# Optimization experiments

Measured on AMD Instinct MI355X. Metric: run time of the kernel, lower is better.

Reference implementation:

```python
import jax, jax.numpy as jnp
import numpy as np

B, N, E = 256, 10000, 160000
H1, H2 = 1024, 128


def setup_inputs() -> dict:
    key = jax.random.key(0)
    ks = jax.random.split(key, 8)
    data = jax.random.normal(ks[0], (B, N), dtype=jnp.float32)
    edge_index = jax.random.randint(ks[1], (2, E), 0, N, dtype=jnp.int64)
    # GCNConv(1, 1): scalar weight + scalar bias (Glorot-ish init)
    gcn_w = jax.random.normal(ks[2], (1,), dtype=jnp.float32)
    gcn_b = jnp.zeros((1,), dtype=jnp.float32)
    # encoder: Linear(N, 1024) -> ReLU -> Linear(1024, 128) -> ReLU
    W1 = jax.random.normal(ks[3], (N, H1), dtype=jnp.float32) * (1.0 / np.sqrt(N))
    b1 = jnp.zeros((H1,), dtype=jnp.float32)
    W2 = jax.random.normal(ks[4], (H1, H2), dtype=jnp.float32) * (1.0 / np.sqrt(H1))
    b2 = jnp.zeros((H2,), dtype=jnp.float32)
    return {"data": data, "gcn_w": gcn_w, "gcn_b": gcn_b,
            "W1": W1, "b1": b1, "W2": W2, "b2": b2,
            "edge_index": edge_index}


def reference(data, gcn_w, gcn_b, W1, b1, W2, b2, edge_index):
    n = data.shape[1]
    # PyG GCNConv defaults: add self-loops, symmetric normalization.
    loop = jnp.arange(n, dtype=edge_index.dtype)
    src = jnp.concatenate([edge_index[0], loop])  # [E+N]
    dst = jnp.concatenate([edge_index[1], loop])
    deg = jax.ops.segment_sum(jnp.ones_like(dst, dtype=data.dtype), dst,
                              num_segments=n)  # >= 1 thanks to self-loops
    dinv = jax.lax.rsqrt(deg)
    norm = dinv[src] * dinv[dst]  # [E+N]
    # linear on 1-dim node features == scalar multiply, batched over B samples
    xw = data * gcn_w[0]                      # [B, N]
    msgs = xw[:, src] * norm                  # [B, E+N]
    agg = jax.ops.segment_sum(msgs.T, dst, num_segments=n).T  # [B, N]
    g = jax.nn.relu(agg + gcn_b[0])           # relu'd GCN output, one row per sample
    # dense MLP encoder (p_drop = 0 so dropout is identity)
    h = jax.nn.relu(g @ W1 + b1)              # [B, 1024]
    return jax.nn.relu(h @ W2 + b2)           # [B, 128]
```

## Files before the change

kernel.cpp:

```cpp
#include <hip/hip_runtime.h>
#include <hip/hip_bf16.h>


#define KPAD 10240
#define NSTEPS 20
#define ZSPLIT 16
#define ELLW 64

typedef __attribute__((ext_vector_type(8))) short short8v;
typedef __attribute__((ext_vector_type(4))) float f32x4;

__device__ inline short f2bf(float f) {
    union { float f; unsigned u; } v; v.f = f;
    unsigned r = v.u + 0x7fffu + ((v.u >> 16) & 1u);
    return (short)(r >> 16);
}

__device__ inline float bf2f(short s) {
    union { unsigned u; float f; } v;
    v.u = ((unsigned)(unsigned short)s) << 16;
    return v.f;
}

__device__ inline void gll16(const short* g, short* l) {
    __builtin_amdgcn_global_load_lds(
        (const __attribute__((address_space(1))) void*)g,
        (__attribute__((address_space(3))) void*)l, 16, 0, 0);
}

__global__ void pack_kernel(const float* __restrict__ data, const float* __restrict__ gw,
                            short* __restrict__ xwT, const float* __restrict__ W1,
                            short* __restrict__ W1T, float4* __restrict__ cntz,
                            int N, int B, int H1, int tTiles, int cTiles) {
    __shared__ short tile[32][66];
    int id = blockIdx.x, t = threadIdx.x;
    if (id < tTiles) {
        int nt = (N + 31) >> 5;
        int xb = id % nt, yb = id / nt;
        int n0 = xb * 32, b0 = yb * 32;
        float w = gw[0];
        int tx = t & 31, ty = t >> 5;
#pragma unroll
        for (int i = 0; i < 4; ++i) {
            int b = b0 + ty + i * 8;
            int n = n0 + tx;
            float v = (n < N) ? data[(size_t)b * N + n] : 0.f;
            tile[ty + i * 8][tx] = f2bf(v * w);
        }
        __syncthreads();
#pragma unroll
        for (int i = 0; i < 4; ++i) {
            int n = n0 + ty + i * 8;
            if (n < N) xwT[(size_t)n * B + b0 + tx] = tile[tx][ty + i * 8];
        }
    } else if (id < tTiles + cTiles) {
        int c = id - tTiles;
        int nk = KPAD >> 6;
        int kx = c % nk, hy = c / nk;
        int k0 = kx * 64, h0 = hy * 32;
        int hl = t & 31, kr = t >> 5;
#pragma unroll
        for (int i = 0; i < 8; ++i) {
            int k = k0 + kr + i * 8;
            float v = (k < N) ? W1[(size_t)k * H1 + h0 + hl] : 0.f;
            tile[hl][kr + i * 8] = f2bf(v);
        }
        __syncthreads();
        int kl = t & 63, hr = t >> 6;
#pragma unroll
        for (int i = 0; i < 8; ++i) {
            int h = h0 + hr + i * 4;
            W1T[(size_t)h * KPAD + k0 + kl] = tile[hr + i * 4][kl];
        }
    } else {
        int i = (id - tTiles - cTiles) * 256 + t;
        cntz[i] = make_float4(0.f, 0.f, 0.f, 0.f);
    }
}

__global__ void ell_fill(const int* __restrict__ ei, int* __restrict__ cnt,
                         int* __restrict__ ell, int E) {
    int e = blockIdx.x * blockDim.x + threadIdx.x;
    if (e >= E) return;
    int s = ei[e], d = ei[E + e];
    int c = atomicAdd(&cnt[d], 1);
    if (c < ELLW) ell[(d << 6) + c] = s;
}

__global__ void gather_kernel(const int* __restrict__ cnt, const int* __restrict__ ell,
                              const float* __restrict__ gcn_b, const short* __restrict__ xwT,
                              short* __restrict__ A0, int N, int B) {
    int row = blockIdx.x * 4 + (threadIdx.x >> 6);
    if (row >= N) return;
    int lane = threadIdx.x & 63;
    const short4* x4 = (const short4*)xwT;
    const int B4 = B >> 2;
    float gb = gcn_b[0];
    int dcnt = cnt[row];
    float di = rsqrtf((float)dcnt + 1.0f);
    float w = di * di;
    short4 v = x4[(size_t)row * B4 + lane];
    float ax = bf2f(v.x) * w, ay = bf2f(v.y) * w, az = bf2f(v.z) * w, aw = bf2f(v.w) * w;
    const int* er = ell + ((size_t)row << 6);
    int m = dcnt < ELLW ? dcnt : ELLW;
    int i = 0;
    for (; i + 1 < m; i += 2) {
        int s0 = er[i], s1 = er[i + 1];
        float n0 = rsqrtf((float)cnt[s0] + 1.0f) * di;
        float n1 = rsqrtf((float)cnt[s1] + 1.0f) * di;
        short4 u0 = x4[(size_t)s0 * B4 + lane];
        short4 u1 = x4[(size_t)s1 * B4 + lane];
        ax = fmaf(bf2f(u0.x), n0, ax); ay = fmaf(bf2f(u0.y), n0, ay);
        az = fmaf(bf2f(u0.z), n0, az); aw = fmaf(bf2f(u0.w), n0, aw);
        ax = fmaf(bf2f(u1.x), n1, ax); ay = fmaf(bf2f(u1.y), n1, ay);
        az = fmaf(bf2f(u1.z), n1, az); aw = fmaf(bf2f(u1.w), n1, aw);
    }
    if (i < m) {
        int s0 = er[i];
        float n0 = rsqrtf((float)cnt[s0] + 1.0f) * di;
        short4 u0 = x4[(size_t)s0 * B4 + lane];
        ax = fmaf(bf2f(u0.x), n0, ax); ay = fmaf(bf2f(u0.y), n0, ay);
        az = fmaf(bf2f(u0.z), n0, az); aw = fmaf(bf2f(u0.w), n0, aw);
    }
    short4 s4;
    s4.x = f2bf(fmaxf(ax + gb, 0.f));
    s4.y = f2bf(fmaxf(ay + gb, 0.f));
    s4.z = f2bf(fmaxf(az + gb, 0.f));
    s4.w = f2bf(fmaxf(aw + gb, 0.f));
    ((short4*)(A0 + (size_t)row * B))[lane] = s4;
}

__global__ void convertA(const short* __restrict__ A0, short* __restrict__ A, int K, int M) {
    __shared__ short tile[32][34];
    int k0 = blockIdx.x * 32, m0 = blockIdx.y * 32;
    int tx = threadIdx.x, ty = threadIdx.y;
#pragma unroll
    for (int i = 0; i < 4; ++i) {
        int k = k0 + ty + i * 8;
        short v = (k < K) ? A0[(size_t)k * M + m0 + tx] : (short)0;
        tile[tx][ty + i * 8] = v;
    }
    __syncthreads();
#pragma unroll
    for (int i = 0; i < 4; ++i) {
        int m = m0 + ty + i * 8;
        A[(size_t)m * KPAD + k0 + tx] = tile[ty + i * 8][tx];
    }
}

__global__ void __launch_bounds__(512)
gemm1_mfma(const short* __restrict__ A, const short* __restrict__ Wt,
           float* __restrict__ hpart) {
    __shared__ __align__(16) short ldsA[2][4096];
    __shared__ __align__(16) short ldsB[2][4096];
    const int n0 = blockIdx.x * 128;
    const int m0 = blockIdx.y * 128;
    const int kz = blockIdx.z * (NSTEPS * 32);
    const int t = threadIdx.x;
    const int l = t & 63, w = t >> 6;
    const int wm = w >> 2, wn = w & 3;
    const int q = l >> 4, i16 = l & 15;

    const int sRow = t & 127, sKq = t >> 7;
    const short* gA = A + (size_t)(m0 + sRow) * KPAD + kz + sKq * 8;
    const short* gB = Wt + (size_t)(n0 + sRow) * KPAD + kz + sKq * 8;
    const int ldst = w * 512;

    f32x4 acc[4][2];
#pragma unroll
    for (int mi = 0; mi < 4; ++mi)
#pragma unroll
        for (int ni = 0; ni < 2; ++ni) acc[mi][ni] = (f32x4){0.f, 0.f, 0.f, 0.f};

    gll16(gA, &ldsA[0][ldst]);
    gll16(gB, &ldsB[0][ldst]);
    gA += 32; gB += 32;

    for (int ks = 0; ks < NSTEPS; ++ks) {
        const int cur = ks & 1;
        if (ks + 1 < NSTEPS) {
            gll16(gA, &ldsA[cur ^ 1][ldst]);
            gll16(gB, &ldsB[cur ^ 1][ldst]);
            gA += 32; gB += 32;
            asm volatile("s_waitcnt vmcnt(2)" ::: "memory");
        } else {
            asm volatile("s_waitcnt vmcnt(0)" ::: "memory");
        }
        __builtin_amdgcn_s_barrier();
        __builtin_amdgcn_sched_barrier(0);
        const short* bA = &ldsA[cur][0];
        const short* bB = &ldsB[cur][0];
        short8v a[4], b[2];
#pragma unroll
        for (int mi = 0; mi < 4; ++mi)
            a[mi] = *(const short8v*)&bA[q * 1024 + (wm * 64 + mi * 16 + i16) * 8];
#pragma unroll
        for (int ni = 0; ni < 2; ++ni)
            b[ni] = *(const short8v*)&bB[q * 1024 + (wn * 32 + ni * 16 + i16) * 8];
#pragma unroll
        for (int mi = 0; mi < 4; ++mi)
#pragma unroll
            for (int ni = 0; ni < 2; ++ni)
                acc[mi][ni] = __builtin_amdgcn_mfma_f32_16x16x32_bf16(a[mi], b[ni], acc[mi][ni], 0, 0, 0);
        __builtin_amdgcn_s_barrier();
    }

    float* hp = hpart + (size_t)blockIdx.z * (256 * 1024);
#pragma unroll
    for (int mi = 0; mi < 4; ++mi) {
#pragma unroll
        for (int ni = 0; ni < 2; ++ni) {
#pragma unroll
            for (int r = 0; r < 4; ++r) {
                int mr = m0 + wm * 64 + mi * 16 + q * 4 + r;
                int nc = n0 + wn * 32 + ni * 16 + i16;
                hp[(size_t)mr * 1024 + nc] = acc[mi][ni][r];
            }
        }
    }
}

__global__ void gemm2_fused(const float* __restrict__ hpart, const float* __restrict__ b1,
                            const float* __restrict__ W2, const float* __restrict__ b2,
                            float* __restrict__ out, int Z) {
    __shared__ float h_lds[1024];
    __shared__ float partial[8][128];
    int b = blockIdx.x, t = threadIdx.x;
    float s = 0.f;
    for (int z = 0; z < Z; ++z) s += hpart[(size_t)z * (256 * 1024) + b * 1024 + t];
    h_lds[t] = fmaxf(s + b1[t], 0.f);
    __syncthreads();
    int j = t & 127, oct = t >> 7;
    const float* w2p = W2 + (size_t)oct * 128 * 128 + j;
    const float* hp = h_lds + oct * 128;
    float s0 = 0.f, s1 = 0.f, s2 = 0.f, s3 = 0.f;
#pragma unroll 8
    for (int k = 0; k < 128; k += 4) {
        s0 = fmaf(hp[k],     w2p[(size_t)k * 128],       s0);
        s1 = fmaf(hp[k + 1], w2p[(size_t)(k + 1) * 128], s1);
        s2 = fmaf(hp[k + 2], w2p[(size_t)(k + 2) * 128], s2);
        s3 = fmaf(hp[k + 3], w2p[(size_t)(k + 3) * 128], s3);
    }
    partial[oct][j] = (s0 + s1) + (s2 + s3);
    __syncthreads();
    if (t < 128) {
        float v = b2[t];
#pragma unroll
        for (int o = 0; o < 8; ++o) v += partial[o][t];
        out[(size_t)b * 128 + t] = fmaxf(v, 0.f);
    }
}

extern "C" void kernel_launch(void* const* d_in, const int* in_sizes, int n_in,
                              void* d_out, int out_size, void* d_ws, size_t ws_size,
                              hipStream_t stream) {
    const float* data = (const float*)d_in[0];
    const float* gw   = (const float*)d_in[1];
    const float* gb   = (const float*)d_in[2];
    const float* W1   = (const float*)d_in[3];
    const float* b1   = (const float*)d_in[4];
    const float* W2   = (const float*)d_in[5];
    const float* b2   = (const float*)d_in[6];
    const int*   ei   = (const int*)d_in[7];
    float* out = (float*)d_out;

    const int B  = 256;
    const int H1 = in_sizes[4];
    const int H2 = in_sizes[6];
    const int N  = in_sizes[3] / H1;
    const int E  = in_sizes[7] / 2;
    const int NP = 10240;

    int* iws = (int*)d_ws;
    int*   cnt  = iws;
    int*   ell  = cnt + NP;
    short* S    = (short*)(ell + (size_t)NP * ELLW);
    short* A    = S;
    short* W1T  = A + (size_t)256 * KPAD;
    short* xwT  = W1T + (size_t)1024 * KPAD;
    short* A0   = xwT + (size_t)N * B;
    float* hpart = (float*)xwT;

    const int tTiles = ((N + 31) / 32) * (B / 32);
    const int cTiles = (KPAD / 64) * (H1 / 32);
    const int zBlks  = NP / 1024;

    pack_kernel<<<tTiles + cTiles + zBlks, 256, 0, stream>>>(
        data, gw, xwT, W1, W1T, (float4*)cnt, N, B, H1, tTiles, cTiles);

    ell_fill<<<(E + 255) / 256, 256, 0, stream>>>(ei, cnt, ell, E);

    gather_kernel<<<(N + 3) / 4, 256, 0, stream>>>(cnt, ell, gb, xwT, A0, N, B);

    convertA<<<dim3(KPAD / 32, B / 32), dim3(32, 8), 0, stream>>>(A0, A, N, B);

    dim3 g1(H1 / 128, B / 128, ZSPLIT);
    gemm1_mfma<<<g1, 512, 0, stream>>>(A, W1T, hpart);

    gemm2_fused<<<B, 1024, 0, stream>>>(hpart, b1, W2, b2, out, ZSPLIT);
}
```

Measured before the change: 90.65 us.

## Deepen GEMM1 K tile, unroll gather by four, batch four rows in GEMM2

GEMM1 now stages 64 K elements per pipeline step instead of 32. This halves the number of barrier-synchronised iterations and doubles LDS buffers, while keeping the same K range per z-split. The gather loop is unrolled by four to issue more independent neighbour loads. GEMM2 processes four batch rows per block so each W2 element is loaded once for four rows, using a quarter as many blocks. The costs are higher LDS use, which can reduce GEMM1 occupancy, and less parallelism in GEMM2.

```diff
diff --git a/kernel.cpp b/kernel.cpp
--- a/kernel.cpp
+++ b/kernel.cpp
@@ -3,7 +3,7 @@
 
 
 #define KPAD 10240
-#define NSTEPS 20
+#define NSTEPS 10
 #define ZSPLIT 16
 #define ELLW 64
 
@@ -104,6 +104,25 @@
     const int* er = ell + ((size_t)row << 6);
     int m = dcnt < ELLW ? dcnt : ELLW;
     int i = 0;
+    for (; i + 3 < m; i += 4) {
+        int s0 = er[i], s1 = er[i + 1], s2 = er[i + 2], s3 = er[i + 3];
+        float n0 = rsqrtf((float)cnt[s0] + 1.0f) * di;
+        float n1 = rsqrtf((float)cnt[s1] + 1.0f) * di;
+        float n2 = rsqrtf((float)cnt[s2] + 1.0f) * di;
+        float n3 = rsqrtf((float)cnt[s3] + 1.0f) * di;
+        short4 u0 = x4[(size_t)s0 * B4 + lane];
+        short4 u1 = x4[(size_t)s1 * B4 + lane];
+        short4 u2 = x4[(size_t)s2 * B4 + lane];
+        short4 u3 = x4[(size_t)s3 * B4 + lane];
+        ax = fmaf(bf2f(u0.x), n0, ax); ay = fmaf(bf2f(u0.y), n0, ay);
+        az = fmaf(bf2f(u0.z), n0, az); aw = fmaf(bf2f(u0.w), n0, aw);
+        ax = fmaf(bf2f(u1.x), n1, ax); ay = fmaf(bf2f(u1.y), n1, ay);
+        az = fmaf(bf2f(u1.z), n1, az); aw = fmaf(bf2f(u1.w), n1, aw);
+        ax = fmaf(bf2f(u2.x), n2, ax); ay = fmaf(bf2f(u2.y), n2, ay);
+        az = fmaf(bf2f(u2.z), n2, az); aw = fmaf(bf2f(u2.w), n2, aw);
+        ax = fmaf(bf2f(u3.x), n3, ax); ay = fmaf(bf2f(u3.y), n3, ay);
+        az = fmaf(bf2f(u3.z), n3, az); aw = fmaf(bf2f(u3.w), n3, aw);
+    }
     for (; i + 1 < m; i += 2) {
         int s0 = er[i], s1 = er[i + 1];
         float n0 = rsqrtf((float)cnt[s0] + 1.0f) * di;
@@ -151,11 +170,11 @@
 __global__ void __launch_bounds__(512)
 gemm1_mfma(const short* __restrict__ A, const short* __restrict__ Wt,
            float* __restrict__ hpart) {
-    __shared__ __align__(16) short ldsA[2][4096];
-    __shared__ __align__(16) short ldsB[2][4096];
+    __shared__ __align__(16) short ldsA[2][8192];
+    __shared__ __align__(16) short ldsB[2][8192];
     const int n0 = blockIdx.x * 128;
     const int m0 = blockIdx.y * 128;
-    const int kz = blockIdx.z * (NSTEPS * 32);
+    const int kz = blockIdx.z * (NSTEPS * 64);
     const int t = threadIdx.x;
     const int l = t & 63, w = t >> 6;
     const int wm = w >> 2, wn = w & 3;
@@ -164,7 +183,8 @@
     const int sRow = t & 127, sKq = t >> 7;
     const short* gA = A + (size_t)(m0 + sRow) * KPAD + kz + sKq * 8;
     const short* gB = Wt + (size_t)(n0 + sRow) * KPAD + kz + sKq * 8;
-    const int ldst = w * 512;
+    const int ld0 = w * 512;
+    const int ld1 = 4096 + w * 512;
 
     f32x4 acc[4][2];
 #pragma unroll
@@ -172,17 +192,17 @@
 #pragma unroll
         for (int ni = 0; ni < 2; ++ni) acc[mi][ni] = (f32x4){0.f, 0.f, 0.f, 0.f};
 
-    gll16(gA, &ldsA[0][ldst]);
-    gll16(gB, &ldsB[0][ldst]);
-    gA += 32; gB += 32;
+    gll16(gA, &ldsA[0][ld0]); gll16(gA + 32, &ldsA[0][ld1]);
+    gll16(gB, &ldsB[0][ld0]); gll16(gB + 32, &ldsB[0][ld1]);
+    gA += 64; gB += 64;
 
     for (int ks = 0; ks < NSTEPS; ++ks) {
         const int cur = ks & 1;
         if (ks + 1 < NSTEPS) {
-            gll16(gA, &ldsA[cur ^ 1][ldst]);
-            gll16(gB, &ldsB[cur ^ 1][ldst]);
-            gA += 32; gB += 32;
-            asm volatile("s_waitcnt vmcnt(2)" ::: "memory");
+            gll16(gA, &ldsA[cur ^ 1][ld0]); gll16(gA + 32, &ldsA[cur ^ 1][ld1]);
+            gll16(gB, &ldsB[cur ^ 1][ld0]); gll16(gB + 32, &ldsB[cur ^ 1][ld1]);
+            gA += 64; gB += 64;
+            asm volatile("s_waitcnt vmcnt(4)" ::: "memory");
         } else {
             asm volatile("s_waitcnt vmcnt(0)" ::: "memory");
         }
@@ -190,18 +210,22 @@
         __builtin_amdgcn_sched_barrier(0);
         const short* bA = &ldsA[cur][0];
         const short* bB = &ldsB[cur][0];
-        short8v a[4], b[2];
-#pragma unroll
-        for (int mi = 0; mi < 4; ++mi)
-            a[mi] = *(const short8v*)&bA[q * 1024 + (wm * 64 + mi * 16 + i16) * 8];
-#pragma unroll
-        for (int ni = 0; ni < 2; ++ni)
-            b[ni] = *(const short8v*)&bB[q * 1024 + (wn * 32 + ni * 16 + i16) * 8];
-#pragma unroll
-        for (int mi = 0; mi < 4; ++mi)
+#pragma unroll
+        for (int kh = 0; kh < 2; ++kh) {
+            const int kq = kh * 4 + q;
+            short8v a[4], b[2];
+#pragma unroll
+            for (int mi = 0; mi < 4; ++mi)
+                a[mi] = *(const short8v*)&bA[kq * 1024 + (wm * 64 + mi * 16 + i16) * 8];
 #pragma unroll
             for (int ni = 0; ni < 2; ++ni)
-                acc[mi][ni] = __builtin_amdgcn_mfma_f32_16x16x32_bf16(a[mi], b[ni], acc[mi][ni], 0, 0, 0);
+                b[ni] = *(const short8v*)&bB[kq * 1024 + (wn * 32 + ni * 16 + i16) * 8];
+#pragma unroll
+            for (int mi = 0; mi < 4; ++mi)
+#pragma unroll
+                for (int ni = 0; ni < 2; ++ni)
+                    acc[mi][ni] = __builtin_amdgcn_mfma_f32_16x16x32_bf16(a[mi], b[ni], acc[mi][ni], 0, 0, 0);
+        }
         __builtin_amdgcn_s_barrier();
     }
 
@@ -223,31 +247,40 @@
 __global__ void gemm2_fused(const float* __restrict__ hpart, const float* __restrict__ b1,
                             const float* __restrict__ W2, const float* __restrict__ b2,
                             float* __restrict__ out, int Z) {
-    __shared__ float h_lds[1024];
-    __shared__ float partial[8][128];
-    int b = blockIdx.x, t = threadIdx.x;
-    float s = 0.f;
-    for (int z = 0; z < Z; ++z) s += hpart[(size_t)z * (256 * 1024) + b * 1024 + t];
-    h_lds[t] = fmaxf(s + b1[t], 0.f);
+    __shared__ float h_lds[4][1024];
+    __shared__ float partial[8][4][128];
+    int b0 = blockIdx.x * 4, t = threadIdx.x;
+#pragma unroll
+    for (int i = 0; i < 4; ++i) {
+        int e = t + i * 1024;
+        int row = e >> 10, col = e & 1023;
+        float s = 0.f;
+        for (int z = 0; z < Z; ++z)
+            s += hpart[(size_t)z * (256 * 1024) + (size_t)(b0 + row) * 1024 + col];
+        h_lds[row][col] = fmaxf(s + b1[col], 0.f);
+    }
     __syncthreads();
     int j = t & 127, oct = t >> 7;
     const float* w2p = W2 + (size_t)oct * 128 * 128 + j;
-    const float* hp = h_lds + oct * 128;
+    const float* hp = &h_lds[0][oct * 128];
     float s0 = 0.f, s1 = 0.f, s2 = 0.f, s3 = 0.f;
-#pragma unroll 8
-    for (int k = 0; k < 128; k += 4) {
-        s0 = fmaf(hp[k],     w2p[(size_t)k * 128],       s0);
-        s1 = fmaf(hp[k + 1], w2p[(size_t)(k + 1) * 128], s1);
-        s2 = fmaf(hp[k + 2], w2p[(size_t)(k + 2) * 128], s2);
-        s3 = fmaf(hp[k + 3], w2p[(size_t)(k + 3) * 128], s3);
-    }
-    partial[oct][j] = (s0 + s1) + (s2 + s3);
+#pragma unroll 4
+    for (int k = 0; k < 128; ++k) {
+        float wv = w2p[(size_t)k * 128];
+        s0 = fmaf(hp[k],        wv, s0);
+        s1 = fmaf(hp[k + 1024], wv, s1);
+        s2 = fmaf(hp[k + 2048], wv, s2);
+        s3 = fmaf(hp[k + 3072], wv, s3);
+    }
+    partial[oct][0][j] = s0; partial[oct][1][j] = s1;
+    partial[oct][2][j] = s2; partial[oct][3][j] = s3;
     __syncthreads();
-    if (t < 128) {
-        float v = b2[t];
-#pragma unroll
-        for (int o = 0; o < 8; ++o) v += partial[o][t];
-        out[(size_t)b * 128 + t] = fmaxf(v, 0.f);
+    if (t < 512) {
+        int row = t >> 7, jj = t & 127;
+        float v = b2[jj];
+#pragma unroll
+        for (int o = 0; o < 8; ++o) v += partial[o][row][jj];
+        out[(size_t)(b0 + row) * 128 + jj] = fmaxf(v, 0.f);
     }
 }
 
@@ -297,5 +330,5 @@
     dim3 g1(H1 / 128, B / 128, ZSPLIT);
     gemm1_mfma<<<g1, 512, 0, stream>>>(A, W1T, hpart);
 
-    gemm2_fused<<<B, 1024, 0, stream>>>(hpart, b1, W2, b2, out, ZSPLIT);
-}
+    gemm2_fused<<<B / 4, 1024, 0, stream>>>(hpart, b1, W2, b2, out, ZSPLIT);
+}
```

Result: slower. 99.58 us (+9.9%).
